# Kernel optimization log

Hardware: AMD Instinct MI355X
Metric: run time of the kernel (lower is better)

## Reference

```python
import jax, jax.numpy as jnp
import numpy as np

D_MODEL = 256; N_LAYERS = 4; INPUT_LEN = 15
D_INNER = 512; D_STATE = 16; D_CONV = 4; DT_RANK = 16
BATCH = 4; SEQ = 2048; EPS = 1e-5

def _ln(x, w, b):
    m = jnp.mean(x, -1, keepdims=True)
    v = jnp.var(x, -1, keepdims=True)
    return (x - m) * jax.lax.rsqrt(v + EPS) * w + b

def _silu(x):
    return x * jax.nn.sigmoid(x)

def _mixer(h, inW, cw, cb, xpW, dtW, dtb, A_log, Dp, opW):
    # h: [B,L,d_model]
    xz = h @ inW.T                      # [B,L,2*D_INNER]
    xh, z = jnp.split(xz, 2, axis=-1)
    # causal depthwise conv1d
    xc = jnp.transpose(xh, (0, 2, 1))   # [B,D,L]
    xc = jax.lax.conv_general_dilated(xc, cw, (1,), [(D_CONV - 1, 0)],
                                      feature_group_count=D_INNER,
                                      dimension_numbers=('NCH', 'OIH', 'NCH'))
    xc = xc + cb[None, :, None]
    xh = _silu(jnp.transpose(xc, (0, 2, 1)))  # [B,L,D]
    dbl = xh @ xpW.T                    # [B,L,DT_RANK+2N]
    dt = dbl[..., :DT_RANK]
    Bm = dbl[..., DT_RANK:DT_RANK + D_STATE]
    C = dbl[..., DT_RANK + D_STATE:]
    dt = jax.nn.softplus(dt @ dtW.T + dtb)    # [B,L,D]
    A = -jnp.exp(A_log)                       # [D,N]
    dA = jnp.exp(dt[..., None] * A)           # [B,L,D,N]
    dBu = dt[..., None] * Bm[:, :, None, :] * xh[..., None]  # [B,L,D,N]
    def step(hst, inp):
        dA_t, dBu_t, C_t = inp
        hst = dA_t * hst + dBu_t
        y = jnp.einsum('bdn,bn->bd', hst, C_t)
        return hst, y
    h0 = jnp.zeros((xh.shape[0], D_INNER, D_STATE), xh.dtype)
    _, ys = jax.lax.scan(step, h0, (jnp.transpose(dA, (1, 0, 2, 3)),
                                    jnp.transpose(dBu, (1, 0, 2, 3)),
                                    jnp.transpose(C, (1, 0, 2))))
    y = jnp.transpose(ys, (1, 0, 2)) + Dp * xh
    y = y * _silu(z)
    return y @ opW.T

def setup_inputs():
    key = jax.random.key(0)
    ks = jax.random.split(key, 8)
    s = 0.02
    return {
        'x_src': jax.random.normal(ks[0], (BATCH, SEQ, INPUT_LEN), jnp.float32),
        'single_eval_pos': 1024,
        'in_W': jax.random.normal(ks[1], (D_MODEL, INPUT_LEN)) * s,
        'norm_w': jnp.ones((N_LAYERS, D_MODEL)),
        'norm_b': jnp.zeros((N_LAYERS, D_MODEL)),
        'inproj_W': jax.random.normal(ks[2], (N_LAYERS, 2 * D_INNER, D_MODEL)) * s,
        'conv_w': jax.random.normal(ks[3], (N_LAYERS, D_INNER, 1, D_CONV)) * 0.2,
        'conv_b': jnp.zeros((N_LAYERS, D_INNER)),
        'xproj_W': jax.random.normal(ks[4], (N_LAYERS, DT_RANK + 2 * D_STATE, D_INNER)) * s,
        'dtproj_W': jax.random.normal(ks[5], (N_LAYERS, D_INNER, DT_RANK)) * 0.1,
        'dtproj_b': jnp.log(jnp.expm1(jnp.full((N_LAYERS, D_INNER), 0.01))),
        'A_log': jnp.log(jnp.broadcast_to(jnp.arange(1, D_STATE + 1, dtype=jnp.float32), (N_LAYERS, D_INNER, D_STATE)) + 0.0),
        'D_param': jnp.ones((N_LAYERS, D_INNER)),
        'outproj_W': jax.random.normal(ks[6], (N_LAYERS, D_MODEL, D_INNER)) * s,
        'out_W': jax.random.normal(ks[7], (1, D_MODEL)) * s,
    }

def reference(x_src, single_eval_pos, in_W, norm_w, norm_b, inproj_W, conv_w, conv_b, xproj_W, dtproj_W, dtproj_b, A_log, D_param, outproj_W, out_W):
    h = x_src @ in_W.T                  # [B,L,d_model]
    res = None
    for i in range(N_LAYERS):
        res = h if res is None else h + res
        hn = _ln(res, norm_w[i], norm_b[i])
        h = _mixer(hn, inproj_W[i], conv_w[i], conv_b[i], xproj_W[i],
                   dtproj_W[i], dtproj_b[i], A_log[i], D_param[i], outproj_W[i])
    # backbone returns hidden_states directly (norm_f defined but not applied)
    return h @ out_W.T                  # [B,L,1]
```

## Files before the change

### kernel.cpp

```cpp
#include <hip/hip_runtime.h>

#define B_   4
#define T_   2048
#define BT_  8192
#define INL  15
#define DM   256
#define DI   512
#define DX   1024
#define DS_  16
#define DR_  16
#define NO_  48
#define NL   4
#define NC_  128
#define LCH  16

typedef short bf16x8 __attribute__((ext_vector_type(8)));
typedef float f32x4  __attribute__((ext_vector_type(4)));

__device__ __forceinline__ float sigmoidf_(float x){
    return __builtin_amdgcn_rcpf(1.f + __expf(-x));
}
__device__ __forceinline__ float softplusf_(float x){
    return fmaxf(x, 0.f) + __logf(1.f + __expf(-fabsf(x)));
}

__device__ __forceinline__ unsigned short f2bf(float x){
    union { float f; unsigned u; } v; v.f = x;
    unsigned r = (v.u + 0x7FFFu + ((v.u >> 16) & 1u)) >> 16;
    return (unsigned short)r;
}
__device__ __forceinline__ float bf2f(unsigned short h){
    union { unsigned u; float f; } v; v.u = ((unsigned)h) << 16;
    return v.f;
}

__device__ __forceinline__ void ld16(const float* __restrict__ p, float* v){
    const float4* q = (const float4*)p;
    float4 x0=q[0],x1=q[1],x2=q[2],x3=q[3];
    v[0]=x0.x; v[1]=x0.y; v[2]=x0.z; v[3]=x0.w;
    v[4]=x1.x; v[5]=x1.y; v[6]=x1.z; v[7]=x1.w;
    v[8]=x2.x; v[9]=x2.y; v[10]=x2.z; v[11]=x2.w;
    v[12]=x3.x; v[13]=x3.y; v[14]=x3.z; v[15]=x3.w;
}
__device__ __forceinline__ void st16(float* __restrict__ p, const float* v){
    float4* q = (float4*)p;
    q[0] = make_float4(v[0],v[1],v[2],v[3]);
    q[1] = make_float4(v[4],v[5],v[6],v[7]);
    q[2] = make_float4(v[8],v[9],v[10],v[11]);
    q[3] = make_float4(v[12],v[13],v[14],v[15]);
}

__global__ void k_cvtW3(const float* __restrict__ W0, unsigned short* __restrict__ h0,
                        unsigned short* __restrict__ l0, int n0,
                        const float* __restrict__ W1, unsigned short* __restrict__ h1,
                        unsigned short* __restrict__ l1, int n1,
                        const float* __restrict__ W2, unsigned short* __restrict__ h2,
                        unsigned short* __restrict__ l2, int n2){
    int g = blockIdx.x*256 + threadIdx.x;
    const float* W; unsigned short *hi, *lo; int idx;
    if(g < n0){ W = W0; hi = h0; lo = l0; idx = g; }
    else if(g < n0+n1){ W = W1; hi = h1; lo = l1; idx = g - n0; }
    else if(g < n0+n1+n2){ W = W2; hi = h2; lo = l2; idx = g - n0 - n1; }
    else return;
    float4 v = ((const float4*)W)[idx];
    ushort4 h, l;
    h.x = f2bf(v.x); l.x = f2bf(v.x - bf2f(h.x));
    h.y = f2bf(v.y); l.y = f2bf(v.y - bf2f(h.y));
    h.z = f2bf(v.z); l.z = f2bf(v.z - bf2f(h.z));
    h.w = f2bf(v.w); l.w = f2bf(v.w - bf2f(h.w));
    ((ushort4*)hi)[idx] = h;
    ((ushort4*)lo)[idx] = l;
}

__global__ void k_inln(const float* __restrict__ x, const float* __restrict__ W,
                       float* __restrict__ res,
                       unsigned short* __restrict__ hnhi, unsigned short* __restrict__ hnlo,
                       const float* __restrict__ w, const float* __restrict__ b){
    int wv = threadIdx.x >> 6, lane = threadIdx.x & 63;
    int bt = blockIdx.x*4 + wv;
    const float* xr = x + bt*INL;
    float xl[INL];
#pragma unroll
    for(int k=0;k<INL;k++) xl[k] = xr[k];
    float4 v;
    float* vv = (float*)&v;
#pragma unroll
    for(int j=0;j<4;j++){
        int m = lane*4 + j;
        const float* wr = W + m*INL;
        float acc = 0.f;
#pragma unroll
        for(int k=0;k<INL;k++) acc += xl[k]*wr[k];
        vv[j] = acc;
    }
    ((float4*)(res + (size_t)bt*DM))[lane] = v;
    float s  = v.x+v.y+v.z+v.w;
    float ss = v.x*v.x+v.y*v.y+v.z*v.z+v.w*v.w;
#pragma unroll
    for(int m=1;m<64;m<<=1){ s += __shfl_xor(s,m); ss += __shfl_xor(ss,m); }
    float mean = s*(1.f/DM);
    float var  = ss*(1.f/DM) - mean*mean;
    float inv  = rsqrtf(var + 1e-5f);
    float4 wt = ((const float4*)w)[lane];
    float4 bs = ((const float4*)b)[lane];
    float4 o;
    o.x = (v.x-mean)*inv*wt.x + bs.x;
    o.y = (v.y-mean)*inv*wt.y + bs.y;
    o.z = (v.z-mean)*inv*wt.z + bs.z;
    o.w = (v.w-mean)*inv*wt.w + bs.w;
    ushort4 hh, ll;
    hh.x = f2bf(o.x); ll.x = f2bf(o.x - bf2f(hh.x));
    hh.y = f2bf(o.y); ll.y = f2bf(o.y - bf2f(hh.y));
    hh.z = f2bf(o.z); ll.z = f2bf(o.z - bf2f(hh.z));
    hh.w = f2bf(o.w); ll.w = f2bf(o.w - bf2f(hh.w));
    ((ushort4*)(hnhi + (size_t)bt*DM))[lane] = hh;
    ((ushort4*)(hnlo + (size_t)bt*DM))[lane] = ll;
}

__global__ void k_resln(const float* __restrict__ h, float* __restrict__ res,
                        unsigned short* __restrict__ hnhi, unsigned short* __restrict__ hnlo,
                        const float* __restrict__ w, const float* __restrict__ b, int addRes){
    int wv = threadIdx.x >> 6, lane = threadIdx.x & 63;
    int bt = blockIdx.x*4 + wv;
    float4 v = ((const float4*)(h + (size_t)bt*DM))[lane];
    if(addRes){
        float4 r = ((const float4*)(res + (size_t)bt*DM))[lane];
        v.x+=r.x; v.y+=r.y; v.z+=r.z; v.w+=r.w;
    }
    ((float4*)(res + (size_t)bt*DM))[lane] = v;
    float s  = v.x+v.y+v.z+v.w;
    float ss = v.x*v.x+v.y*v.y+v.z*v.z+v.w*v.w;
#pragma unroll
    for(int m=1;m<64;m<<=1){ s += __shfl_xor(s,m); ss += __shfl_xor(ss,m); }
    float mean = s*(1.f/DM);
    float var  = ss*(1.f/DM) - mean*mean;
    float inv  = rsqrtf(var + 1e-5f);
    float4 wt = ((const float4*)w)[lane];
    float4 bs = ((const float4*)b)[lane];
    float4 o;
    o.x = (v.x-mean)*inv*wt.x + bs.x;
    o.y = (v.y-mean)*inv*wt.y + bs.y;
    o.z = (v.z-mean)*inv*wt.z + bs.z;
    o.w = (v.w-mean)*inv*wt.w + bs.w;
    ushort4 hh, ll;
    hh.x = f2bf(o.x); ll.x = f2bf(o.x - bf2f(hh.x));
    hh.y = f2bf(o.y); ll.y = f2bf(o.y - bf2f(hh.y));
    hh.z = f2bf(o.z); ll.z = f2bf(o.z - bf2f(hh.z));
    hh.w = f2bf(o.w); ll.w = f2bf(o.w - bf2f(hh.w));
    ((ushort4*)(hnhi + (size_t)bt*DM))[lane] = hh;
    ((ushort4*)(hnlo + (size_t)bt*DM))[lane] = ll;
}

template<int BM,int BN>
__global__ void __launch_bounds__(256) k_gemm_bf3(
    const unsigned short* __restrict__ Ahi, const unsigned short* __restrict__ Alo,
    const unsigned short* __restrict__ Bhi, const unsigned short* __restrict__ Blo,
    float* __restrict__ C, int M, int N, int K)
{
    constexpr int LDP = 40;
    constexpr int WM = BM/2, WN = BN/2;
    constexpr int MI_ = WM/16, NI_ = WN/16;
    __shared__ unsigned short sAh[BM*LDP], sAl[BM*LDP], sBh[BN*LDP], sBl[BN*LDP];
    int tid  = threadIdx.x;
    int wave = tid >> 6, lane = tid & 63;
    int wm0  = (wave >> 1) * WM, wn0 = (wave & 1) * WN;
    int m0   = blockIdx.y * BM, n0 = blockIdx.x * BN;
    int lr   = lane & 15;
    int kq   = (lane >> 4) * 8;
    int quad4 = (lane >> 4) * 4;

    f32x4 acc[MI_][NI_];
#pragma unroll
    for(int i=0;i<MI_;i++)
#pragma unroll
        for(int j=0;j<NI_;j++) acc[i][j] = (f32x4){0.f,0.f,0.f,0.f};

    for(int k0=0;k0<K;k0+=32){
#pragma unroll
        for(int i=tid;i<BM*4;i+=256){
            int r = i>>2, cg = (i&3)*8;
            size_t go = (size_t)(m0+r)*K + k0 + cg;
            *(float4*)(&sAh[r*LDP + cg]) = *(const float4*)(Ahi + go);
            *(float4*)(&sAl[r*LDP + cg]) = *(const float4*)(Alo + go);
        }
#pragma unroll
        for(int i=tid;i<BN*4;i+=256){
            int r = i>>2, cg = (i&3)*8;
            size_t go = (size_t)(n0+r)*K + k0 + cg;
            *(float4*)(&sBh[r*LDP + cg]) = *(const float4*)(Bhi + go);
            *(float4*)(&sBl[r*LDP + cg]) = *(const float4*)(Blo + go);
        }
        __syncthreads();
        bf16x8 ah[MI_], al[MI_], bh[NI_], bl[NI_];
#pragma unroll
        for(int mi=0;mi<MI_;mi++){
            int ro = (wm0 + mi*16 + lr)*LDP + kq;
            ah[mi] = *(const bf16x8*)(&sAh[ro]);
            al[mi] = *(const bf16x8*)(&sAl[ro]);
        }
#pragma unroll
        for(int ni=0;ni<NI_;ni++){
            int ro = (wn0 + ni*16 + lr)*LDP + kq;
            bh[ni] = *(const bf16x8*)(&sBh[ro]);
            bl[ni] = *(const bf16x8*)(&sBl[ro]);
        }
#pragma unroll
        for(int mi=0;mi<MI_;mi++)
#pragma unroll
            for(int ni=0;ni<NI_;ni++){
                acc[mi][ni] = __builtin_amdgcn_mfma_f32_16x16x32_bf16(ah[mi], bh[ni], acc[mi][ni], 0,0,0);
                acc[mi][ni] = __builtin_amdgcn_mfma_f32_16x16x32_bf16(ah[mi], bl[ni], acc[mi][ni], 0,0,0);
                acc[mi][ni] = __builtin_amdgcn_mfma_f32_16x16x32_bf16(al[mi], bh[ni], acc[mi][ni], 0,0,0);
            }
        __syncthreads();
    }
#pragma unroll
    for(int mi=0;mi<MI_;mi++)
#pragma unroll
        for(int ni=0;ni<NI_;ni++){
            int col = n0 + wn0 + ni*16 + lr;
#pragma unroll
            for(int r=0;r<4;r++){
                int row = m0 + wm0 + mi*16 + quad4 + r;
                C[(size_t)row*N + col] = acc[mi][ni][r];
            }
        }
}

template<int BM,int BN>
__global__ void __launch_bounds__(256) k_gemm_pk(
    const unsigned* __restrict__ Apk,
    const unsigned short* __restrict__ Bhi, const unsigned short* __restrict__ Blo,
    float* __restrict__ C, int M, int N, int K)
{
    constexpr int LDP = 40;
    constexpr int WM = BM/2, WN = BN/2;
    constexpr int MI_ = WM/16, NI_ = WN/16;
    __shared__ unsigned short sAh[BM*LDP], sAl[BM*LDP], sBh[BN*LDP], sBl[BN*LDP];
    int tid  = threadIdx.x;
    int wave = tid >> 6, lane = tid & 63;
    int wm0  = (wave >> 1) * WM, wn0 = (wave & 1) * WN;
    int m0   = blockIdx.y * BM, n0 = blockIdx.x * BN;
    int lr   = lane & 15;
    int kq   = (lane >> 4) * 8;
    int quad4 = (lane >> 4) * 4;

    f32x4 acc[MI_][NI_];
#pragma unroll
    for(int i=0;i<MI_;i++)
#pragma unroll
        for(int j=0;j<NI_;j++) acc[i][j] = (f32x4){0.f,0.f,0.f,0.f};

    for(int k0=0;k0<K;k0+=32){
#pragma unroll
        for(int i=tid;i<BM*2;i+=256){
            int r = i>>1, hf = (i&1)*16;
            const uint4* yp = (const uint4*)(Apk + (size_t)(m0+r)*K + k0 + hf);
#pragma unroll
            for(int q=0;q<4;q++){
                uint4 p = yp[q];
                ushort4 H, L;
                H.x=(unsigned short)p.x;  L.x=(unsigned short)(p.x>>16);
                H.y=(unsigned short)p.y;  L.y=(unsigned short)(p.y>>16);
                H.z=(unsigned short)p.z;  L.z=(unsigned short)(p.z>>16);
                H.w=(unsigned short)p.w;  L.w=(unsigned short)(p.w>>16);
                *(ushort4*)(&sAh[r*LDP + hf + q*4]) = H;
                *(ushort4*)(&sAl[r*LDP + hf + q*4]) = L;
            }
        }
#pragma unroll
        for(int i=tid;i<BN*4;i+=256){
            int r = i>>2, cg = (i&3)*8;
            size_t go = (size_t)(n0+r)*K + k0 + cg;
            *(float4*)(&sBh[r*LDP + cg]) = *(const float4*)(Bhi + go);
            *(float4*)(&sBl[r*LDP + cg]) = *(const float4*)(Blo + go);
        }
        __syncthreads();
        bf16x8 ah[MI_], al[MI_], bh[NI_], bl[NI_];
#pragma unroll
        for(int mi=0;mi<MI_;mi++){
            int ro = (wm0 + mi*16 + lr)*LDP + kq;
            ah[mi] = *(const bf16x8*)(&sAh[ro]);
            al[mi] = *(const bf16x8*)(&sAl[ro]);
        }
#pragma unroll
        for(int ni=0;ni<NI_;ni++){
            int ro = (wn0 + ni*16 + lr)*LDP + kq;
            bh[ni] = *(const bf16x8*)(&sBh[ro]);
            bl[ni] = *(const bf16x8*)(&sBl[ro]);
        }
#pragma unroll
        for(int mi=0;mi<MI_;mi++)
#pragma unroll
            for(int ni=0;ni<NI_;ni++){
                acc[mi][ni] = __builtin_amdgcn_mfma_f32_16x16x32_bf16(ah[mi], bh[ni], acc[mi][ni], 0,0,0);
                acc[mi][ni] = __builtin_amdgcn_mfma_f32_16x16x32_bf16(ah[mi], bl[ni], acc[mi][ni], 0,0,0);
                acc[mi][ni] = __builtin_amdgcn_mfma_f32_16x16x32_bf16(al[mi], bh[ni], acc[mi][ni], 0,0,0);
            }
        __syncthreads();
    }
#pragma unroll
    for(int mi=0;mi<MI_;mi++)
#pragma unroll
        for(int ni=0;ni<NI_;ni++){
            int col = n0 + wn0 + ni*16 + lr;
#pragma unroll
            for(int r=0;r<4;r++){
                int row = m0 + wm0 + mi*16 + quad4 + r;
                C[(size_t)row*N + col] = acc[mi][ni][r];
            }
        }
}

__global__ void __launch_bounds__(512,4) k_convxp2(
    const float* __restrict__ xz, const float* __restrict__ cw, const float* __restrict__ cb,
    const unsigned short* __restrict__ Bhi, const unsigned short* __restrict__ Blo,
    const float* __restrict__ dtW, const float* __restrict__ dtbias,
    const float* __restrict__ A_log,
    float* __restrict__ xh, float* __restrict__ dbl,
    float* __restrict__ S, float* __restrict__ sdt)
{
    __shared__ unsigned short sAh[16*520], sAl[16*520];
    __shared__ float sP[6][16][20];
    __shared__ float sXh[16*512];
    __shared__ float sD[16*52];

    int tid = threadIdx.x;
    int wave = tid >> 6, lane = tid & 63;
    int lr = lane & 15, kq = (lane>>4)*8, quad4 = (lane>>4)*4;
    int m0 = blockIdx.x * LCH;
    int d  = tid;
    int nt = wave >> 1, kh = wave & 1;

    float xv[19];
    {
        int rbase = m0 - 3;
        bool mask0 = ((m0 & (T_-1)) == 0);
#pragma unroll
        for(int j=0;j<19;j++)
            xv[j] = (mask0 && j<3) ? 0.f : xz[(size_t)(rbase+j)*DX + d];
    }
    bf16x8 pbh[8], pbl[8];
    if(wave < 6){
        const unsigned short* bhp = Bhi + (size_t)(nt*16 + lr)*DI + kh*256 + kq;
        const unsigned short* blp = Blo + (size_t)(nt*16 + lr)*DI + kh*256 + kq;
#pragma unroll
        for(int ks=0;ks<8;ks++){
            pbh[ks] = *(const bf16x8*)(bhp + ks*32);
            pbl[ks] = *(const bf16x8*)(blp + ks*32);
        }
    }
    float4 w4 = *(const float4*)(cw + d*4);
    float bias = cb[d];
#pragma unroll
    for(int t=0;t<16;t++){
        float a = bias + w4.x*xv[t] + w4.y*xv[t+1] + w4.z*xv[t+2] + w4.w*xv[t+3];
        float v = a * sigmoidf_(a);
        xh[(size_t)(m0+t)*DI + d] = v;
        sXh[t*512 + d] = v;
        unsigned short hh = f2bf(v);
        sAh[t*520 + d] = hh;
        sAl[t*520 + d] = f2bf(v - bf2f(hh));
    }
    float a_[16]; ld16(A_log + (size_t)d*16, a_);
#pragma unroll
    for(int n=0;n<16;n++) a_[n] = -__expf(a_[n]);
    float wr_[16]; ld16(dtW + (size_t)d*16, wr_);
    float bsv = dtbias[d];
    __syncthreads();

    if(wave < 6){
        f32x4 acc = {0.f,0.f,0.f,0.f};
#pragma unroll
        for(int ks=0;ks<8;ks++){
            int ao = lr*520 + kh*256 + ks*32 + kq;
            bf16x8 ah = *(const bf16x8*)(&sAh[ao]);
            bf16x8 al = *(const bf16x8*)(&sAl[ao]);
            acc = __builtin_amdgcn_mfma_f32_16x16x32_bf16(ah, pbh[ks], acc, 0,0,0);
            acc = __builtin_amdgcn_mfma_f32_16x16x32_bf16(ah, pbl[ks], acc, 0,0,0);
            acc = __builtin_amdgcn_mfma_f32_16x16x32_bf16(al, pbh[ks], acc, 0,0,0);
        }
#pragma unroll
        for(int r=0;r<4;r++) sP[wave][quad4+r][lr] = acc[r];
    }
    __syncthreads();

    for(int i=tid;i<768;i+=512){
        int t = i/48, n = i - t*48;
        int nt2 = n >> 4, nn = n & 15;
        float v = sP[nt2*2][t][nn] + sP[nt2*2+1][t][nn];
        dbl[(size_t)(m0+t)*48 + n] = v;
        sD[t*52 + n] = v;
    }
    __syncthreads();

    int b = m0 >> 11;
    int c = (m0 & (T_-1)) >> 4;
    float st_[16];
#pragma unroll
    for(int n=0;n<16;n++) st_[n] = 0.f;
    float sd = 0.f;
#pragma unroll 4
    for(int t=0;t<16;t++){
        float dl[16]; ld16(&sD[t*52], dl);
        float bv[16]; ld16(&sD[t*52 + 16], bv);
        float pre = bsv;
#pragma unroll
        for(int r=0;r<16;r++) pre += dl[r]*wr_[r];
        float dtv = softplusf_(pre);
        float xhv = sXh[t*512 + d];
        float dx = dtv*xhv;
        sd += dtv;
#pragma unroll
        for(int n=0;n<16;n++) st_[n] = __expf(dtv*a_[n])*st_[n] + dx*bv[n];
    }
    st16(S + (((size_t)b*NC_ + c)*DI + d)*16, st_);
    sdt[((size_t)b*NC_ + c)*DI + d] = sd;
}

__global__ void k_scan2(const float* __restrict__ S, const float* __restrict__ sdt,
                        const float* __restrict__ A_log, float* __restrict__ Hinit){
    int g = blockIdx.x*256 + threadIdx.x;
    int b = g >> 13;
    int dn = g & 8191;
    int d = dn >> 4;
    float a = -__expf(A_log[dn]);
    float H = 0.f;
    for(int c0=0;c0<NC_;c0+=8){
        float sv[8], gv[8];
#pragma unroll
        for(int j=0;j<8;j++){
            sv[j] = S[((size_t)(b*NC_ + c0 + j))*8192 + dn];
            gv[j] = sdt[(size_t)(b*NC_ + c0 + j)*DI + d];
        }
#pragma unroll
        for(int j=0;j<8;j++){
            size_t o = ((size_t)(b*NC_ + c0 + j))*8192 + dn;
            Hinit[o] = H;
            H = __expf(gv[j]*a)*H + sv[j];
        }
    }
}

__global__ void __launch_bounds__(256) k_scan3(
    const float* __restrict__ dbl, const float* __restrict__ xh, const float* __restrict__ xz,
    const float* __restrict__ A_log, const float* __restrict__ Dpar,
    const float* __restrict__ dtW, const float* __restrict__ dtbias,
    const float* __restrict__ Hinit, unsigned* __restrict__ Y)
{
    __shared__ float sbc[16*52];
    int tid = threadIdx.x;
    int c = blockIdx.y, b = blockIdx.z;
    int m0 = b*T_ + c*LCH;
    if(tid < 192){
        int t = tid/12, s = tid - t*12;
        *(float4*)(&sbc[t*52 + s*4]) = *(const float4*)(dbl + (size_t)(m0+t)*48 + s*4);
    }
    __syncthreads();
    int d = blockIdx.x*256 + tid;
    float xhp[16], zvp[16];
#pragma unroll
    for(int t=0;t<16;t++){
        xhp[t] = xh[(size_t)(m0+t)*DI + d];
        zvp[t] = xz[(size_t)(m0+t)*DX + DI + d];
    }
    float a_[16]; ld16(A_log + (size_t)d*16, a_);
#pragma unroll
    for(int n=0;n<16;n++) a_[n] = -__expf(a_[n]);
    float wr_[16]; ld16(dtW + (size_t)d*16, wr_);
    float bsv = dtbias[d];
    float st_[16]; ld16(Hinit + (((size_t)b*NC_ + c)*DI + d)*16, st_);
    float Dp = Dpar[d];
#pragma unroll 2
    for(int t=0;t<LCH;t++){
        int bt = m0 + t;
        float dl[16]; ld16(&sbc[t*52], dl);
        float bv[16]; ld16(&sbc[t*52 + 16], bv);
        float cv[16]; ld16(&sbc[t*52 + 32], cv);
        float pre = bsv;
#pragma unroll
        for(int r=0;r<16;r++) pre += dl[r]*wr_[r];
        float dtv = softplusf_(pre);
        float xhv = xhp[t];
        float dx = dtv*xhv;
        float y = 0.f;
#pragma unroll
        for(int n=0;n<16;n++){
            st_[n] = __expf(dtv*a_[n])*st_[n] + dx*bv[n];
            y += st_[n]*cv[n];
        }
        float zv = zvp[t];
        y += Dp*xhv;
        y = y * zv * sigmoidf_(zv);
        unsigned short hh = f2bf(y);
        unsigned short ll = f2bf(y - bf2f(hh));
        Y[(size_t)bt*DI + d] = (unsigned)hh | ((unsigned)ll << 16);
    }
}

__global__ void k_outw(const float* __restrict__ h, const float* __restrict__ ow,
                       float* __restrict__ out){
    int wv = threadIdx.x >> 6, lane = threadIdx.x & 63;
    int bt = blockIdx.x*4 + wv;
    float4 v = ((const float4*)(h + (size_t)bt*DM))[lane];
    float4 w = ((const float4*)ow)[lane];
    float s = v.x*w.x + v.y*w.y + v.z*w.z + v.w*w.w;
#pragma unroll
    for(int m=1;m<64;m<<=1) s += __shfl_xor(s,m);
    if(lane==0) out[bt] = s;
}

extern "C" void kernel_launch(void* const* d_in, const int* in_sizes, int n_in,
                              void* d_out, int out_size, void* d_ws, size_t ws_size,
                              hipStream_t stream){
    const float* x_src    = (const float*)d_in[0];
    const float* in_W     = (const float*)d_in[2];
    const float* norm_w   = (const float*)d_in[3];
    const float* norm_b   = (const float*)d_in[4];
    const float* inproj_W = (const float*)d_in[5];
    const float* conv_w   = (const float*)d_in[6];
    const float* conv_b   = (const float*)d_in[7];
    const float* xproj_W  = (const float*)d_in[8];
    const float* dtproj_W = (const float*)d_in[9];
    const float* dtproj_b = (const float*)d_in[10];
    const float* A_log    = (const float*)d_in[11];
    const float* D_param  = (const float*)d_in[12];
    const float* outproj_W= (const float*)d_in[13];
    const float* out_W    = (const float*)d_in[14];

    float* ws  = (float*)d_ws;
    float* h    = ws;
    float* res  = h    + (size_t)BT_*DM;
    float* xz   = res  + (size_t)BT_*DM;
    float* xh   = xz   + (size_t)BT_*DX;
    float* dbl  = xh   + (size_t)BT_*DI;
    float* sdtb = dbl  + (size_t)BT_*48;
    float* Sbuf = sdtb + (size_t)B_*NC_*DI;
    float* Hbuf = Sbuf + (size_t)B_*NC_*DI*DS_;
    unsigned short* us = (unsigned short*)(Hbuf + (size_t)B_*NC_*DI*DS_);
    unsigned short* WhiIn  = us;
    unsigned short* WloIn  = WhiIn  + (size_t)NL*DX*DM;
    unsigned short* WhiOut = WloIn  + (size_t)NL*DX*DM;
    unsigned short* WloOut = WhiOut + (size_t)NL*DM*DI;
    unsigned short* WhiXp  = WloOut + (size_t)NL*DM*DI;
    unsigned short* WloXp  = WhiXp  + (size_t)NL*NO_*DI;
    unsigned short* hnhi   = WloXp  + (size_t)NL*NO_*DI;
    unsigned short* hnlo   = hnhi   + (size_t)BT_*DM;
    unsigned*       ybuf   = (unsigned*)(hnlo + (size_t)BT_*DM);

    int n0 = NL*DX*DM/4, n1 = NL*DM*DI/4, n2 = NL*NO_*DI/4;
    k_cvtW3<<<(n0+n1+n2 + 255)/256, 256, 0, stream>>>(
        inproj_W,  WhiIn,  WloIn,  n0,
        outproj_W, WhiOut, WloOut, n1,
        xproj_W,   WhiXp,  WloXp,  n2);
    k_inln<<<BT_/4, 256, 0, stream>>>(x_src, in_W, res, hnhi, hnlo, norm_w, norm_b);
    for(int i=0;i<NL;i++){
        if(i > 0)
            k_resln<<<BT_/4, 256, 0, stream>>>(h, res, hnhi, hnlo, norm_w + i*DM, norm_b + i*DM, 1);
        k_gemm_bf3<128,128><<<dim3(DX/128, BT_/128), 256, 0, stream>>>(
            hnhi, hnlo, WhiIn + (size_t)i*DX*DM, WloIn + (size_t)i*DX*DM, xz, BT_, DX, DM);
        k_convxp2<<<BT_/LCH, 512, 0, stream>>>(xz, conv_w + i*DI*4, conv_b + i*DI,
            WhiXp + (size_t)i*NO_*DI, WloXp + (size_t)i*NO_*DI,
            dtproj_W + (size_t)i*DI*DR_, dtproj_b + i*DI,
            A_log + (size_t)i*DI*DS_, xh, dbl, Sbuf, sdtb);
        k_scan2<<<B_*DI*DS_/256, 256, 0, stream>>>(Sbuf, sdtb, A_log + (size_t)i*DI*DS_, Hbuf);
        k_scan3<<<dim3(2, NC_, B_), 256, 0, stream>>>(dbl, xh, xz,
            A_log + (size_t)i*DI*DS_, D_param + i*DI,
            dtproj_W + (size_t)i*DI*DR_, dtproj_b + i*DI, Hbuf, ybuf);
        k_gemm_pk<128,64><<<dim3(DM/64, BT_/128), 256, 0, stream>>>(
            ybuf, WhiOut + (size_t)i*DM*DI, WloOut + (size_t)i*DM*DI, h, BT_, DM, DI);
    }
    k_outw<<<BT_/4, 256, 0, stream>>>(h, out_W, (float*)d_out);
}
```

Measured before the change: 596.6 us.

## Fold final out_proj and output head into one GEMV; trim convxp2 registers

The last layer's out_proj GEMM followed by the out_W projection is replaced with a precomputed combined weight vector (out_W @ outproj_W[3]) and a single GEMV over the packed y buffer. This removes the final [8192x512]x[512x256] GEMM. Separately, k_convxp2 drops its occupancy launch bound and the sXh shared buffer, keeps the xh values in registers, and loads the xproj B fragments inside the MFMA loop instead of prefetching them all. That trades register pressure for more global and L2 loads.

```diff
diff --git a/kernel.cpp b/kernel.cpp
--- a/kernel.cpp
+++ b/kernel.cpp
@@ -72,6 +72,15 @@
     ((ushort4*)lo)[idx] = l;
 }
 
+__global__ void k_wcomb(const float* __restrict__ opW, const float* __restrict__ outW,
+                        float* __restrict__ cw){
+    int k = blockIdx.x*256 + threadIdx.x;
+    float s = 0.f;
+#pragma unroll 8
+    for(int m=0;m<DM;m++) s += outW[m]*opW[(size_t)m*DI + k];
+    cw[k] = s;
+}
+
 __global__ void k_inln(const float* __restrict__ x, const float* __restrict__ W,
                        float* __restrict__ res,
                        unsigned short* __restrict__ hnhi, unsigned short* __restrict__ hnlo,
@@ -312,7 +321,7 @@
         }
 }
 
-__global__ void __launch_bounds__(512,4) k_convxp2(
+__global__ void __launch_bounds__(512) k_convxp2(
     const float* __restrict__ xz, const float* __restrict__ cw, const float* __restrict__ cb,
     const unsigned short* __restrict__ Bhi, const unsigned short* __restrict__ Blo,
     const float* __restrict__ dtW, const float* __restrict__ dtbias,
@@ -322,7 +331,6 @@
 {
     __shared__ unsigned short sAh[16*520], sAl[16*520];
     __shared__ float sP[6][16][20];
-    __shared__ float sXh[16*512];
     __shared__ float sD[16*52];
 
     int tid = threadIdx.x;
@@ -340,45 +348,38 @@
         for(int j=0;j<19;j++)
             xv[j] = (mask0 && j<3) ? 0.f : xz[(size_t)(rbase+j)*DX + d];
     }
-    bf16x8 pbh[8], pbl[8];
+    float a_[16]; ld16(A_log + (size_t)d*16, a_);
+    float wr_[16]; ld16(dtW + (size_t)d*16, wr_);
+    float bsv = dtbias[d];
+    float4 w4 = *(const float4*)(cw + d*4);
+    float bias = cb[d];
+    float vh[16];
+#pragma unroll
+    for(int t=0;t<16;t++){
+        float a = bias + w4.x*xv[t] + w4.y*xv[t+1] + w4.z*xv[t+2] + w4.w*xv[t+3];
+        float v = a * sigmoidf_(a);
+        vh[t] = v;
+        xh[(size_t)(m0+t)*DI + d] = v;
+        unsigned short hh = f2bf(v);
+        sAh[t*520 + d] = hh;
+        sAl[t*520 + d] = f2bf(v - bf2f(hh));
+    }
+    __syncthreads();
+
     if(wave < 6){
         const unsigned short* bhp = Bhi + (size_t)(nt*16 + lr)*DI + kh*256 + kq;
         const unsigned short* blp = Blo + (size_t)(nt*16 + lr)*DI + kh*256 + kq;
-#pragma unroll
-        for(int ks=0;ks<8;ks++){
-            pbh[ks] = *(const bf16x8*)(bhp + ks*32);
-            pbl[ks] = *(const bf16x8*)(blp + ks*32);
-        }
-    }
-    float4 w4 = *(const float4*)(cw + d*4);
-    float bias = cb[d];
-#pragma unroll
-    for(int t=0;t<16;t++){
-        float a = bias + w4.x*xv[t] + w4.y*xv[t+1] + w4.z*xv[t+2] + w4.w*xv[t+3];
-        float v = a * sigmoidf_(a);
-        xh[(size_t)(m0+t)*DI + d] = v;
-        sXh[t*512 + d] = v;
-        unsigned short hh = f2bf(v);
-        sAh[t*520 + d] = hh;
-        sAl[t*520 + d] = f2bf(v - bf2f(hh));
-    }
-    float a_[16]; ld16(A_log + (size_t)d*16, a_);
-#pragma unroll
-    for(int n=0;n<16;n++) a_[n] = -__expf(a_[n]);
-    float wr_[16]; ld16(dtW + (size_t)d*16, wr_);
-    float bsv = dtbias[d];
-    __syncthreads();
-
-    if(wave < 6){
         f32x4 acc = {0.f,0.f,0.f,0.f};
-#pragma unroll
+#pragma unroll 4
         for(int ks=0;ks<8;ks++){
             int ao = lr*520 + kh*256 + ks*32 + kq;
             bf16x8 ah = *(const bf16x8*)(&sAh[ao]);
             bf16x8 al = *(const bf16x8*)(&sAl[ao]);
-            acc = __builtin_amdgcn_mfma_f32_16x16x32_bf16(ah, pbh[ks], acc, 0,0,0);
-            acc = __builtin_amdgcn_mfma_f32_16x16x32_bf16(ah, pbl[ks], acc, 0,0,0);
-            acc = __builtin_amdgcn_mfma_f32_16x16x32_bf16(al, pbh[ks], acc, 0,0,0);
+            bf16x8 bh = *(const bf16x8*)(bhp + ks*32);
+            bf16x8 bl = *(const bf16x8*)(blp + ks*32);
+            acc = __builtin_amdgcn_mfma_f32_16x16x32_bf16(ah, bh, acc, 0,0,0);
+            acc = __builtin_amdgcn_mfma_f32_16x16x32_bf16(ah, bl, acc, 0,0,0);
+            acc = __builtin_amdgcn_mfma_f32_16x16x32_bf16(al, bh, acc, 0,0,0);
         }
 #pragma unroll
         for(int r=0;r<4;r++) sP[wave][quad4+r][lr] = acc[r];
@@ -394,6 +395,8 @@
     }
     __syncthreads();
 
+#pragma unroll
+    for(int n=0;n<16;n++) a_[n] = -__expf(a_[n]);
     int b = m0 >> 11;
     int c = (m0 & (T_-1)) >> 4;
     float st_[16];
@@ -408,8 +411,7 @@
 #pragma unroll
         for(int r=0;r<16;r++) pre += dl[r]*wr_[r];
         float dtv = softplusf_(pre);
-        float xhv = sXh[t*512 + d];
-        float dx = dtv*xhv;
+        float dx = dtv*vh[t];
         sd += dtv;
 #pragma unroll
         for(int n=0;n<16;n++) st_[n] = __expf(dtv*a_[n])*st_[n] + dx*bv[n];
@@ -498,13 +500,22 @@
     }
 }
 
-__global__ void k_outw(const float* __restrict__ h, const float* __restrict__ ow,
+__global__ void k_gemv(const unsigned* __restrict__ Y, const float* __restrict__ cw,
                        float* __restrict__ out){
     int wv = threadIdx.x >> 6, lane = threadIdx.x & 63;
     int bt = blockIdx.x*4 + wv;
-    float4 v = ((const float4*)(h + (size_t)bt*DM))[lane];
-    float4 w = ((const float4*)ow)[lane];
-    float s = v.x*w.x + v.y*w.y + v.z*w.z + v.w*w.w;
+    const uint4* yp = (const uint4*)(Y + (size_t)bt*DI);
+    uint4 p0 = yp[lane*2], p1 = yp[lane*2+1];
+    float4 c0 = ((const float4*)cw)[lane*2], c1 = ((const float4*)cw)[lane*2+1];
+    float s = 0.f;
+    s += (bf2f((unsigned short)p0.x) + bf2f((unsigned short)(p0.x>>16))) * c0.x;
+    s += (bf2f((unsigned short)p0.y) + bf2f((unsigned short)(p0.y>>16))) * c0.y;
+    s += (bf2f((unsigned short)p0.z) + bf2f((unsigned short)(p0.z>>16))) * c0.z;
+    s += (bf2f((unsigned short)p0.w) + bf2f((unsigned short)(p0.w>>16))) * c0.w;
+    s += (bf2f((unsigned short)p1.x) + bf2f((unsigned short)(p1.x>>16))) * c1.x;
+    s += (bf2f((unsigned short)p1.y) + bf2f((unsigned short)(p1.y>>16))) * c1.y;
+    s += (bf2f((unsigned short)p1.z) + bf2f((unsigned short)(p1.z>>16))) * c1.z;
+    s += (bf2f((unsigned short)p1.w) + bf2f((unsigned short)(p1.w>>16))) * c1.w;
 #pragma unroll
     for(int m=1;m<64;m<<=1) s += __shfl_xor(s,m);
     if(lane==0) out[bt] = s;
@@ -547,12 +558,14 @@
     unsigned short* hnhi   = WloXp  + (size_t)NL*NO_*DI;
     unsigned short* hnlo   = hnhi   + (size_t)BT_*DM;
     unsigned*       ybuf   = (unsigned*)(hnlo + (size_t)BT_*DM);
+    float*          cwb    = (float*)(ybuf + (size_t)BT_*DI);
 
     int n0 = NL*DX*DM/4, n1 = NL*DM*DI/4, n2 = NL*NO_*DI/4;
     k_cvtW3<<<(n0+n1+n2 + 255)/256, 256, 0, stream>>>(
         inproj_W,  WhiIn,  WloIn,  n0,
         outproj_W, WhiOut, WloOut, n1,
         xproj_W,   WhiXp,  WloXp,  n2);
+    k_wcomb<<<2, 256, 0, stream>>>(outproj_W + (size_t)3*DM*DI, out_W, cwb);
     k_inln<<<BT_/4, 256, 0, stream>>>(x_src, in_W, res, hnhi, hnlo, norm_w, norm_b);
     for(int i=0;i<NL;i++){
         if(i > 0)
@@ -567,8 +580,9 @@
         k_scan3<<<dim3(2, NC_, B_), 256, 0, stream>>>(dbl, xh, xz,
             A_log + (size_t)i*DI*DS_, D_param + i*DI,
             dtproj_W + (size_t)i*DI*DR_, dtproj_b + i*DI, Hbuf, ybuf);
-        k_gemm_pk<128,64><<<dim3(DM/64, BT_/128), 256, 0, stream>>>(
-            ybuf, WhiOut + (size_t)i*DM*DI, WloOut + (size_t)i*DM*DI, h, BT_, DM, DI);
-    }
-    k_outw<<<BT_/4, 256, 0, stream>>>(h, out_W, (float*)d_out);
-}
+        if(i < NL-1)
+            k_gemm_pk<128,64><<<dim3(DM/64, BT_/128), 256, 0, stream>>>(
+                ybuf, WhiOut + (size_t)i*DM*DI, WloOut + (size_t)i*DM*DI, h, BT_, DM, DI);
+    }
+    k_gemv<<<BT_/4, 256, 0, stream>>>(ybuf, cwb, (float*)d_out);
+}
```

Result: faster. 561.7 us (-5.9%).
